# Optimization experiments

Measured on AMD Instinct MI355X. Metric: run time of the kernel, lower is better.

The kernel has to match this reference:

```python
import jax, jax.numpy as jnp
import numpy as np

L, D, H, V, TMAX = 12, 768, 12, 50257, 1024
HD = D // H


def setup_inputs() -> dict:
    key = jax.random.key(0)
    ks = jax.random.split(key, 10)
    std = 0.02
    inp = {
        "input_ids": jax.random.randint(ks[0], (2, 1024), 0, V),
        "wte": jax.random.normal(ks[1], (V, D), jnp.float32) * std,
        "wpe": jax.random.normal(ks[2], (TMAX, D), jnp.float32) * std,
        "ln1_g": jnp.ones((L, D), jnp.float32),
        "ln1_b": jnp.zeros((L, D), jnp.float32),
        "attn_w": jax.random.normal(ks[3], (L, D, 3 * D), jnp.float32) * std,
        "attn_b": jnp.zeros((L, 3 * D), jnp.float32),
        "proj_w": jax.random.normal(ks[4], (L, D, D), jnp.float32) * std,
        "proj_b": jnp.zeros((L, D), jnp.float32),
        "ln2_g": jnp.ones((L, D), jnp.float32),
        "ln2_b": jnp.zeros((L, D), jnp.float32),
        "fc_w": jax.random.normal(ks[5], (L, D, 4 * D), jnp.float32) * std,
        "fc_b": jnp.zeros((L, 4 * D), jnp.float32),
        "fc2_w": jax.random.normal(ks[6], (L, 4 * D, D), jnp.float32) * std,
        "fc2_b": jnp.zeros((L, D), jnp.float32),
        "lnf_g": jnp.ones((D,), jnp.float32),
        "lnf_b": jnp.zeros((D,), jnp.float32),
    }
    return inp


def _layernorm(x, g, b, eps=1e-5):
    m = x.mean(-1, keepdims=True)
    v = ((x - m) ** 2).mean(-1, keepdims=True)
    return (x - m) * jax.lax.rsqrt(v + eps) * g + b


def reference(input_ids, wte, wpe, ln1_g, ln1_b, attn_w, attn_b, proj_w, proj_b,
              ln2_g, ln2_b, fc_w, fc_b, fc2_w, fc2_b, lnf_g, lnf_b):
    B, T = input_ids.shape
    # dropout is identity in eval mode
    x = wte[input_ids] + wpe[:T]  # [B,T,D]
    causal = jnp.tril(jnp.ones((T, T), bool))
    scale = 1.0 / np.sqrt(HD)

    def block(x, p):
        l1g, l1b, aw, ab, pw, pb, l2g, l2b, fw, fb, f2w, f2b = p
        h = _layernorm(x, l1g, l1b)
        qkv = h @ aw + ab  # [B,T,3D]
        q, k, v = jnp.split(qkv, 3, axis=-1)
        q = q.reshape(B, T, H, HD).transpose(0, 2, 1, 3)  # [B,H,T,HD]
        k = k.reshape(B, T, H, HD).transpose(0, 2, 1, 3)
        v = v.reshape(B, T, H, HD).transpose(0, 2, 1, 3)
        att = jnp.einsum('bhqd,bhkd->bhqk', q, k) * scale
        att = jnp.where(causal, att, -jnp.inf)
        att = jax.nn.softmax(att, axis=-1)
        y = jnp.einsum('bhqk,bhkd->bhqd', att, v)
        y = y.transpose(0, 2, 1, 3).reshape(B, T, D)
        x = x + (y @ pw + pb)
        h = _layernorm(x, l2g, l2b)
        h = jax.nn.gelu(h @ fw + fb, approximate=False) @ f2w + f2b
        return x + h, None

    params = (ln1_g, ln1_b, attn_w, attn_b, proj_w, proj_b,
              ln2_g, ln2_b, fc_w, fc_b, fc2_w, fc2_b)
    x, _ = jax.lax.scan(block, x, params)
    x = _layernorm(x, lnf_g, lnf_b)
    logits = x @ wte.T  # tied lm_head, [B,T,V]
    return logits
```

## Files before the change

### kernel.cpp

```cpp
#include <hip/hip_runtime.h>

#define NL 12
#define Dm 768
#define NH 12
#define HD 64
#define NV 50257
#define NB 2
#define NT 1024
#define MROWS (NB * NT)

typedef __attribute__((ext_vector_type(8))) short bf16x8;
typedef __attribute__((ext_vector_type(4))) float f32x4;

__device__ __forceinline__ void split2(float f, unsigned short& h, unsigned short& l) {
    unsigned u = __float_as_uint(f);
    h = (unsigned short)(u >> 16);
    float lf = f - __uint_as_float(u & 0xffff0000u);
    unsigned lu = __float_as_uint(lf);
    l = (unsigned short)((lu + 0x8000u) >> 16);
}

__device__ __forceinline__ float gelu_exact(float v) {
    return 0.5f * v * (1.0f + erff(v * 0.70710678118654752f));
}

union U8 { ushort4 u[2]; bf16x8 v; };

__device__ __forceinline__ bf16x8 ldfrag(const unsigned short* rowp, int lg) {
    U8 t;
    t.u[0] = *(const ushort4*)(rowp + 8 * lg);
    t.u[1] = *(const ushort4*)(rowp + 8 * lg + 4);
    return t.v;
}

__global__ void embed_kernel(const int* __restrict__ ids,
                             const float* __restrict__ wte,
                             const float* __restrict__ wpe,
                             float* __restrict__ x) {
    int row = blockIdx.x;
    int t = row & (NT - 1);
    int id = ids[row];
    const float* src = wte + (size_t)id * Dm;
    const float* pos = wpe + (size_t)t * Dm;
    float* dst = x + (size_t)row * Dm;
    for (int i = threadIdx.x; i < Dm; i += 256)
        dst[i] = src[i] + pos[i];
}

__global__ void ln_kernel(const float* __restrict__ x,
                          const float* __restrict__ g,
                          const float* __restrict__ b,
                          float* __restrict__ out) {
    int row = blockIdx.x;
    int tid = threadIdx.x;
    const float* xr = x + (size_t)row * Dm;
    float v0 = xr[tid];
    float v1 = xr[tid + 256];
    float v2 = xr[tid + 512];
    float s = v0 + v1 + v2;
    #pragma unroll
    for (int off = 32; off; off >>= 1) s += __shfl_xor(s, off);
    __shared__ float red[4];
    __shared__ float red2[4];
    int wid = tid >> 6;
    if ((tid & 63) == 0) red[wid] = s;
    __syncthreads();
    float mean = (red[0] + red[1] + red[2] + red[3]) * (1.0f / Dm);
    float d0 = v0 - mean, d1 = v1 - mean, d2 = v2 - mean;
    float sq = d0 * d0 + d1 * d1 + d2 * d2;
    #pragma unroll
    for (int off = 32; off; off >>= 1) sq += __shfl_xor(sq, off);
    if ((tid & 63) == 0) red2[wid] = sq;
    __syncthreads();
    float var = (red2[0] + red2[1] + red2[2] + red2[3]) * (1.0f / Dm);
    float rstd = rsqrtf(var + 1e-5f);
    float* o = out + (size_t)row * Dm;
    o[tid]       = d0 * rstd * g[tid]       + b[tid];
    o[tid + 256] = d1 * rstd * g[tid + 256] + b[tid + 256];
    o[tid + 512] = d2 * rstd * g[tid + 512] + b[tid + 512];
}

template <int TM, int TN, bool TRANSB>
__global__ __launch_bounds__(256, 3)
void gemm_mfma(const float* __restrict__ A,
               const float* __restrict__ W,
               const float* __restrict__ bias,
               const float* __restrict__ resid,
               float* __restrict__ C,
               int M, int K, int N, int act) {
    constexpr int FRM = TM / 32;
    constexpr int FRN = TN / 32;
    constexpr int CPA = TM / 32;
    constexpr int CPW = TN / 32;
    constexpr int WLD = TN + 4;

    __shared__ __align__(16) unsigned short Ah[TM][36];
    __shared__ __align__(16) unsigned short Al[TM][36];
    __shared__ __align__(16) unsigned short Bh[TN][36];
    __shared__ __align__(16) unsigned short Bl[TN][36];
    __shared__ __align__(16) float Wst[TRANSB ? 4 : 32 * WLD];

    const int tid = threadIdx.x;
    const int lane = tid & 63;
    const int wv = tid >> 6;
    const int wm = wv >> 1, wn = wv & 1;
    const int lr = lane & 15, lg = lane >> 4;
    const int m0 = blockIdx.y * TM;
    const int n0 = blockIdx.x * TN;

    f32x4 acc[FRM][FRN];
    #pragma unroll
    for (int i = 0; i < FRM; ++i)
        #pragma unroll
        for (int j = 0; j < FRN; ++j)
            #pragma unroll
            for (int e = 0; e < 4; ++e) acc[i][j][e] = 0.0f;

    const int ttn = tid & (TN - 1);
    const int tks = (tid / TN) * (TN / 8);

    for (int k0 = 0; k0 < K; k0 += 32) {
        #pragma unroll
        for (int i = 0; i < CPA; ++i) {
            int ci = tid * CPA + i;
            int r = ci >> 3, kc = (ci & 7) << 2;
            float4 v = *(const float4*)(A + (size_t)(m0 + r) * K + k0 + kc);
            ushort4 hh, ll;
            split2(v.x, hh.x, ll.x); split2(v.y, hh.y, ll.y);
            split2(v.z, hh.z, ll.z); split2(v.w, hh.w, ll.w);
            *(ushort4*)&Ah[r][kc] = hh;
            *(ushort4*)&Al[r][kc] = ll;
        }
        if constexpr (TRANSB) {
            #pragma unroll
            for (int i = 0; i < CPW; ++i) {
                int ci = tid * CPW + i;
                int r = ci >> 3, kc = (ci & 7) << 2;
                float4 v = make_float4(0.f, 0.f, 0.f, 0.f);
                if (n0 + r < N)
                    v = *(const float4*)(W + (size_t)(n0 + r) * K + k0 + kc);
                ushort4 hh, ll;
                split2(v.x, hh.x, ll.x); split2(v.y, hh.y, ll.y);
                split2(v.z, hh.z, ll.z); split2(v.w, hh.w, ll.w);
                *(ushort4*)&Bh[r][kc] = hh;
                *(ushort4*)&Bl[r][kc] = ll;
            }
            __syncthreads();
        } else {
            #pragma unroll
            for (int i = 0; i < CPW; ++i) {
                int ci = tid * CPW + i;
                int kk = ci / (TN / 4);
                int nc = (ci % (TN / 4)) << 2;
                *(float4*)&Wst[kk * WLD + nc] =
                    *(const float4*)(W + (size_t)(k0 + kk) * N + n0 + nc);
            }
            __syncthreads();
            #pragma unroll
            for (int j4 = 0; j4 < TN / 32; ++j4) {
                ushort4 hh, ll;
                float w0 = Wst[(tks + j4 * 4 + 0) * WLD + ttn];
                float w1 = Wst[(tks + j4 * 4 + 1) * WLD + ttn];
                float w2 = Wst[(tks + j4 * 4 + 2) * WLD + ttn];
                float w3 = Wst[(tks + j4 * 4 + 3) * WLD + ttn];
                split2(w0, hh.x, ll.x); split2(w1, hh.y, ll.y);
                split2(w2, hh.z, ll.z); split2(w3, hh.w, ll.w);
                *(ushort4*)&Bh[ttn][tks + j4 * 4] = hh;
                *(ushort4*)&Bl[ttn][tks + j4 * 4] = ll;
            }
            __syncthreads();
        }

        bf16x8 afh[FRM], afl[FRM];
        #pragma unroll
        for (int mb = 0; mb < FRM; ++mb) {
            int r = wm * (TM / 2) + mb * 16 + lr;
            afh[mb] = ldfrag(&Ah[r][0], lg);
            afl[mb] = ldfrag(&Al[r][0], lg);
        }
        #pragma unroll
        for (int nb = 0; nb < FRN; ++nb) {
            int cB = wn * (TN / 2) + nb * 16 + lr;
            bf16x8 bfh = ldfrag(&Bh[cB][0], lg);
            bf16x8 bfl = ldfrag(&Bl[cB][0], lg);
            #pragma unroll
            for (int mb = 0; mb < FRM; ++mb) {
                acc[mb][nb] = __builtin_amdgcn_mfma_f32_16x16x32_bf16(afh[mb], bfh, acc[mb][nb], 0, 0, 0);
                acc[mb][nb] = __builtin_amdgcn_mfma_f32_16x16x32_bf16(afl[mb], bfh, acc[mb][nb], 0, 0, 0);
                acc[mb][nb] = __builtin_amdgcn_mfma_f32_16x16x32_bf16(afh[mb], bfl, acc[mb][nb], 0, 0, 0);
            }
        }
        __syncthreads();
    }

    #pragma unroll
    for (int nb = 0; nb < FRN; ++nb) {
        int c = n0 + wn * (TN / 2) + nb * 16 + lr;
        if (c < N) {
            float bv = bias ? bias[c] : 0.0f;
            #pragma unroll
            for (int mb = 0; mb < FRM; ++mb) {
                int rb = m0 + wm * (TM / 2) + mb * 16 + lg * 4;
                #pragma unroll
                for (int i = 0; i < 4; ++i) {
                    size_t idx = (size_t)(rb + i) * N + c;
                    float v = acc[mb][nb][i] + bv;
                    if (act) v = gelu_exact(v);
                    if (resid) v += resid[idx];
                    C[idx] = v;
                }
            }
        }
    }
}

__global__ __launch_bounds__(256, 2)
void attn_mfma(const float* __restrict__ qkv, float* __restrict__ y) {
    __shared__ __align__(16) unsigned short Kh[64][72], Kl[64][72];
    __shared__ __align__(16) unsigned short Vth[64][72], Vtl[64][72];
    __shared__ __align__(16) unsigned short Ph[64][72], Pl[64][72];

    const int tid = threadIdx.x;
    const int lane = tid & 63;
    const int w = tid >> 6;
    const int lr = lane & 15, lg = lane >> 4;
    const int qt = (int)(gridDim.x - 1 - blockIdx.x);
    const int bh = blockIdx.y;
    const int h = bh % NH, b = bh / NH;
    const int q0 = qt * 64;
    const float scale = 0.125f;

    const float* base = qkv + (size_t)b * NT * (3 * Dm);

    bf16x8 qh[2], ql[2];
    {
        const int qrow = q0 + w * 16 + lr;
        const float* qp = base + (size_t)qrow * (3 * Dm) + h * HD + lg * 8;
        #pragma unroll
        for (int ks = 0; ks < 2; ++ks) {
            float4 x0 = *(const float4*)(qp + 32 * ks);
            float4 x1 = *(const float4*)(qp + 32 * ks + 4);
            U8 th, tl;
            split2(x0.x * scale, th.u[0].x, tl.u[0].x);
            split2(x0.y * scale, th.u[0].y, tl.u[0].y);
            split2(x0.z * scale, th.u[0].z, tl.u[0].z);
            split2(x0.w * scale, th.u[0].w, tl.u[0].w);
            split2(x1.x * scale, th.u[1].x, tl.u[1].x);
            split2(x1.y * scale, th.u[1].y, tl.u[1].y);
            split2(x1.z * scale, th.u[1].z, tl.u[1].z);
            split2(x1.w * scale, th.u[1].w, tl.u[1].w);
            qh[ks] = th.v; ql[ks] = tl.v;
        }
    }

    f32x4 yacc[4];
    #pragma unroll
    for (int df = 0; df < 4; ++df)
        #pragma unroll
        for (int e = 0; e < 4; ++e) yacc[df][e] = 0.0f;
    float m[4] = {-1e30f, -1e30f, -1e30f, -1e30f};
    float lsum[4] = {0.0f, 0.0f, 0.0f, 0.0f};

    const int skr = tid >> 4;
    const int sd4 = (tid & 15) << 2;

    for (int kt = 0; kt <= qt; ++kt) {
        const int kt0 = kt * 64;
        __syncthreads();
        #pragma unroll
        for (int i = 0; i < 4; ++i) {
            int kr = i * 16 + skr;
            const float* kp = base + (size_t)(kt0 + kr) * (3 * Dm) + Dm + h * HD + sd4;
            float4 kv = *(const float4*)kp;
            ushort4 hh, ll;
            split2(kv.x, hh.x, ll.x); split2(kv.y, hh.y, ll.y);
            split2(kv.z, hh.z, ll.z); split2(kv.w, hh.w, ll.w);
            *(ushort4*)&Kh[kr][sd4] = hh;
            *(ushort4*)&Kl[kr][sd4] = ll;
            float4 vv = *(const float4*)(kp + Dm);
            unsigned short vh, vl;
            split2(vv.x, vh, vl); Vth[sd4 + 0][kr] = vh; Vtl[sd4 + 0][kr] = vl;
            split2(vv.y, vh, vl); Vth[sd4 + 1][kr] = vh; Vtl[sd4 + 1][kr] = vl;
            split2(vv.z, vh, vl); Vth[sd4 + 2][kr] = vh; Vtl[sd4 + 2][kr] = vl;
            split2(vv.w, vh, vl); Vth[sd4 + 3][kr] = vh; Vtl[sd4 + 3][kr] = vl;
        }
        __syncthreads();

        f32x4 s[4];
        #pragma unroll
        for (int nb = 0; nb < 4; ++nb)
            #pragma unroll
            for (int e = 0; e < 4; ++e) s[nb][e] = 0.0f;
        #pragma unroll
        for (int nb = 0; nb < 4; ++nb) {
            #pragma unroll
            for (int ks = 0; ks < 2; ++ks) {
                bf16x8 kfh = ldfrag(&Kh[nb * 16 + lr][32 * ks], lg);
                bf16x8 kfl = ldfrag(&Kl[nb * 16 + lr][32 * ks], lg);
                s[nb] = __builtin_amdgcn_mfma_f32_16x16x32_bf16(qh[ks], kfh, s[nb], 0, 0, 0);
                s[nb] = __builtin_amdgcn_mfma_f32_16x16x32_bf16(ql[ks], kfh, s[nb], 0, 0, 0);
                s[nb] = __builtin_amdgcn_mfma_f32_16x16x32_bf16(qh[ks], kfl, s[nb], 0, 0, 0);
            }
        }

        if (kt == qt) {
            #pragma unroll
            for (int nb = 0; nb < 4; ++nb) {
                int kg = kt0 + nb * 16 + lr;
                #pragma unroll
                for (int i = 0; i < 4; ++i) {
                    int qg = q0 + w * 16 + 4 * lg + i;
                    if (kg > qg) s[nb][i] = -1e30f;
                }
            }
        }

        float alpha[4];
        #pragma unroll
        for (int i = 0; i < 4; ++i) {
            float mt = fmaxf(fmaxf(s[0][i], s[1][i]), fmaxf(s[2][i], s[3][i]));
            #pragma unroll
            for (int off = 1; off < 16; off <<= 1) mt = fmaxf(mt, __shfl_xor(mt, off));
            float mn = fmaxf(m[i], mt);
            alpha[i] = __expf(m[i] - mn);
            m[i] = mn;
            float rs = 0.0f;
            #pragma unroll
            for (int nb = 0; nb < 4; ++nb) {
                float p = __expf(s[nb][i] - mn);
                s[nb][i] = p;
                rs += p;
            }
            #pragma unroll
            for (int off = 1; off < 16; off <<= 1) rs += __shfl_xor(rs, off);
            lsum[i] = lsum[i] * alpha[i] + rs;
        }

        #pragma unroll
        for (int nb = 0; nb < 4; ++nb) {
            #pragma unroll
            for (int i = 0; i < 4; ++i) {
                unsigned short hh, ll;
                split2(s[nb][i], hh, ll);
                Ph[w * 16 + 4 * lg + i][nb * 16 + lr] = hh;
                Pl[w * 16 + 4 * lg + i][nb * 16 + lr] = ll;
            }
        }
        __syncthreads();

        #pragma unroll
        for (int df = 0; df < 4; ++df)
            #pragma unroll
            for (int i = 0; i < 4; ++i) yacc[df][i] *= alpha[i];
        #pragma unroll
        for (int ks = 0; ks < 2; ++ks) {
            bf16x8 pah = ldfrag(&Ph[w * 16 + lr][32 * ks], lg);
            bf16x8 pal = ldfrag(&Pl[w * 16 + lr][32 * ks], lg);
            #pragma unroll
            for (int df = 0; df < 4; ++df) {
                bf16x8 vfh = ldfrag(&Vth[df * 16 + lr][32 * ks], lg);
                bf16x8 vfl = ldfrag(&Vtl[df * 16 + lr][32 * ks], lg);
                yacc[df] = __builtin_amdgcn_mfma_f32_16x16x32_bf16(pah, vfh, yacc[df], 0, 0, 0);
                yacc[df] = __builtin_amdgcn_mfma_f32_16x16x32_bf16(pal, vfh, yacc[df], 0, 0, 0);
                yacc[df] = __builtin_amdgcn_mfma_f32_16x16x32_bf16(pah, vfl, yacc[df], 0, 0, 0);
            }
        }
    }

    #pragma unroll
    for (int i = 0; i < 4; ++i) {
        float inv = 1.0f / lsum[i];
        int qg = q0 + w * 16 + 4 * lg + i;
        float* yr = y + (size_t)(b * NT + qg) * Dm + h * HD;
        #pragma unroll
        for (int df = 0; df < 4; ++df)
            yr[df * 16 + lr] = yacc[df][i] * inv;
    }
}

extern "C" void kernel_launch(void* const* d_in, const int* in_sizes, int n_in,
                              void* d_out, int out_size, void* d_ws, size_t ws_size,
                              hipStream_t stream) {
    const int*   ids    = (const int*)  d_in[0];
    const float* wte    = (const float*)d_in[1];
    const float* wpe    = (const float*)d_in[2];
    const float* ln1_g  = (const float*)d_in[3];
    const float* ln1_b  = (const float*)d_in[4];
    const float* attn_w = (const float*)d_in[5];
    const float* attn_b = (const float*)d_in[6];
    const float* proj_w = (const float*)d_in[7];
    const float* proj_b = (const float*)d_in[8];
    const float* ln2_g  = (const float*)d_in[9];
    const float* ln2_b  = (const float*)d_in[10];
    const float* fc_w   = (const float*)d_in[11];
    const float* fc_b   = (const float*)d_in[12];
    const float* fc2_w  = (const float*)d_in[13];
    const float* fc2_b  = (const float*)d_in[14];
    const float* lnf_g  = (const float*)d_in[15];
    const float* lnf_b  = (const float*)d_in[16];
    float* out = (float*)d_out;

    float* ws  = (float*)d_ws;
    float* x   = ws;
    float* h   = x   + (size_t)MROWS * Dm;
    float* qkv = h   + (size_t)MROWS * Dm;
    float* y   = qkv + (size_t)MROWS * 3 * Dm;
    float* h4  = y   + (size_t)MROWS * Dm;

    embed_kernel<<<MROWS, 256, 0, stream>>>(ids, wte, wpe, x);

    for (int l = 0; l < NL; ++l) {
        ln_kernel<<<MROWS, 256, 0, stream>>>(x, ln1_g + l * Dm, ln1_b + l * Dm, h);
        gemm_mfma<128, 128, false><<<dim3(3 * Dm / 128, MROWS / 128), 256, 0, stream>>>(
            h, attn_w + (size_t)l * Dm * 3 * Dm, attn_b + (size_t)l * 3 * Dm,
            nullptr, qkv, MROWS, Dm, 3 * Dm, 0);
        attn_mfma<<<dim3(NT / 64, NB * NH), 256, 0, stream>>>(qkv, y);
        gemm_mfma<64, 64, false><<<dim3(Dm / 64, MROWS / 64), 256, 0, stream>>>(
            y, proj_w + (size_t)l * Dm * Dm, proj_b + (size_t)l * Dm,
            x, x, MROWS, Dm, Dm, 0);
        ln_kernel<<<MROWS, 256, 0, stream>>>(x, ln2_g + l * Dm, ln2_b + l * Dm, h);
        gemm_mfma<128, 128, false><<<dim3(4 * Dm / 128, MROWS / 128), 256, 0, stream>>>(
            h, fc_w + (size_t)l * Dm * 4 * Dm, fc_b + (size_t)l * 4 * Dm,
            nullptr, h4, MROWS, Dm, 4 * Dm, 1);
        gemm_mfma<64, 64, false><<<dim3(Dm / 64, MROWS / 64), 256, 0, stream>>>(
            h4, fc2_w + (size_t)l * 4 * Dm * Dm, fc2_b + (size_t)l * Dm,
            x, x, MROWS, 4 * Dm, Dm, 0);
    }

    ln_kernel<<<MROWS, 256, 0, stream>>>(x, lnf_g, lnf_b, h);
    gemm_mfma<128, 128, true><<<dim3((NV + 127) / 128, MROWS / 128), 256, 0, stream>>>(
        h, wte, nullptr, nullptr, out, MROWS, Dm, NV, 0);
}
```

Before: 5.553 ms.

## Pre-split activations and weights into bf16 hi/lo planes outside the GEMM loop

Moves the fp32-to-bf16 hi/lo split out of the GEMM inner loop. Producers (layernorm, attention, the GELU GEMM epilogue) now write split bf16 planes, and weights are pre-split and pre-transposed by separate kernels that run every call. The GEMM then stages ready bf16 tiles straight into shared memory, with no in-loop conversion and no transpose staging. The cost is extra kernels that split all weights each call, plus more workspace traffic from writing and reading hi and lo planes.

```diff
diff --git a/kernel.cpp b/kernel.cpp
--- a/kernel.cpp
+++ b/kernel.cpp
@@ -31,6 +31,39 @@
     t.u[0] = *(const ushort4*)(rowp + 8 * lg);
     t.u[1] = *(const ushort4*)(rowp + 8 * lg + 4);
     return t.v;
+}
+
+__global__ void wtsplit_kernel(const float* __restrict__ W,
+                               unsigned short* __restrict__ Wh,
+                               unsigned short* __restrict__ Wl,
+                               int K, int N) {
+    __shared__ float T[32][33];
+    const int k0 = blockIdx.x * 32, n0 = blockIdx.y * 32;
+    const int t = threadIdx.x;
+    const int r = t >> 3, c4 = (t & 7) << 2;
+    float4 v = *(const float4*)(W + (size_t)(k0 + r) * N + n0 + c4);
+    T[r][c4 + 0] = v.x; T[r][c4 + 1] = v.y; T[r][c4 + 2] = v.z; T[r][c4 + 3] = v.w;
+    __syncthreads();
+    ushort4 hh, ll;
+    split2(T[c4 + 0][r], hh.x, ll.x);
+    split2(T[c4 + 1][r], hh.y, ll.y);
+    split2(T[c4 + 2][r], hh.z, ll.z);
+    split2(T[c4 + 3][r], hh.w, ll.w);
+    *(ushort4*)(Wh + (size_t)(n0 + r) * K + k0 + c4) = hh;
+    *(ushort4*)(Wl + (size_t)(n0 + r) * K + k0 + c4) = ll;
+}
+
+__global__ void wsplit_kernel(const float* __restrict__ W,
+                              unsigned short* __restrict__ Wh,
+                              unsigned short* __restrict__ Wl, size_t n4) {
+    size_t i = (size_t)blockIdx.x * 256 + threadIdx.x;
+    if (i >= n4) return;
+    float4 v = *(const float4*)(W + i * 4);
+    ushort4 hh, ll;
+    split2(v.x, hh.x, ll.x); split2(v.y, hh.y, ll.y);
+    split2(v.z, hh.z, ll.z); split2(v.w, hh.w, ll.w);
+    *(ushort4*)(Wh + i * 4) = hh;
+    *(ushort4*)(Wl + i * 4) = ll;
 }
 
 __global__ void embed_kernel(const int* __restrict__ ids,
@@ -47,10 +80,11 @@
         dst[i] = src[i] + pos[i];
 }
 
-__global__ void ln_kernel(const float* __restrict__ x,
-                          const float* __restrict__ g,
-                          const float* __restrict__ b,
-                          float* __restrict__ out) {
+__global__ void ln_split_kernel(const float* __restrict__ x,
+                                const float* __restrict__ g,
+                                const float* __restrict__ b,
+                                unsigned short* __restrict__ oh,
+                                unsigned short* __restrict__ ol) {
     int row = blockIdx.x;
     int tid = threadIdx.x;
     const float* xr = x + (size_t)row * Dm;
@@ -74,31 +108,33 @@
     __syncthreads();
     float var = (red2[0] + red2[1] + red2[2] + red2[3]) * (1.0f / Dm);
     float rstd = rsqrtf(var + 1e-5f);
-    float* o = out + (size_t)row * Dm;
-    o[tid]       = d0 * rstd * g[tid]       + b[tid];
-    o[tid + 256] = d1 * rstd * g[tid + 256] + b[tid + 256];
-    o[tid + 512] = d2 * rstd * g[tid + 512] + b[tid + 512];
-}
-
-template <int TM, int TN, bool TRANSB>
-__global__ __launch_bounds__(256, 3)
-void gemm_mfma(const float* __restrict__ A,
-               const float* __restrict__ W,
-               const float* __restrict__ bias,
-               const float* __restrict__ resid,
-               float* __restrict__ C,
-               int M, int K, int N, int act) {
+    unsigned short hh, ll;
+    size_t o = (size_t)row * Dm;
+    split2(d0 * rstd * g[tid]       + b[tid],       hh, ll); oh[o + tid]       = hh; ol[o + tid]       = ll;
+    split2(d1 * rstd * g[tid + 256] + b[tid + 256], hh, ll); oh[o + tid + 256] = hh; ol[o + tid + 256] = ll;
+    split2(d2 * rstd * g[tid + 512] + b[tid + 512], hh, ll); oh[o + tid + 512] = hh; ol[o + tid + 512] = ll;
+}
+
+template <int TM, int TN, int BK, bool WSPLIT, bool NGUARD>
+__global__ __launch_bounds__(256, 4)
+void gemm_ps(const unsigned short* __restrict__ Ahg,
+             const unsigned short* __restrict__ Alg,
+             const unsigned short* __restrict__ Whg,
+             const unsigned short* __restrict__ Wlg,
+             const float* __restrict__ Wf,
+             const float* __restrict__ bias,
+             const float* __restrict__ resid,
+             float* __restrict__ C,
+             unsigned short* __restrict__ Ch,
+             unsigned short* __restrict__ Cl,
+             int M, int K, int N, int act) {
+    static_assert(TM * BK == 4096 && TN * BK == 4096, "staging map");
     constexpr int FRM = TM / 32;
     constexpr int FRN = TN / 32;
-    constexpr int CPA = TM / 32;
-    constexpr int CPW = TN / 32;
-    constexpr int WLD = TN + 4;
-
-    __shared__ __align__(16) unsigned short Ah[TM][36];
-    __shared__ __align__(16) unsigned short Al[TM][36];
-    __shared__ __align__(16) unsigned short Bh[TN][36];
-    __shared__ __align__(16) unsigned short Bl[TN][36];
-    __shared__ __align__(16) float Wst[TRANSB ? 4 : 32 * WLD];
+    constexpr int LD = BK + 4;
+
+    __shared__ __align__(16) unsigned short Ahs[TM][LD], Als[TM][LD];
+    __shared__ __align__(16) unsigned short Bhs[TN][LD], Bls[TN][LD];
 
     const int tid = threadIdx.x;
     const int lane = tid & 63;
@@ -108,6 +144,10 @@
     const int m0 = blockIdx.y * TM;
     const int n0 = blockIdx.x * TN;
 
+    constexpr int CPR = BK / 16;
+    const int sr = tid / CPR;
+    const int skc = (tid % CPR) * 16;
+
     f32x4 acc[FRM][FRN];
     #pragma unroll
     for (int i = 0; i < FRM; ++i)
@@ -116,78 +156,77 @@
             #pragma unroll
             for (int e = 0; e < 4; ++e) acc[i][j][e] = 0.0f;
 
-    const int ttn = tid & (TN - 1);
-    const int tks = (tid / TN) * (TN / 8);
-
-    for (int k0 = 0; k0 < K; k0 += 32) {
-        #pragma unroll
-        for (int i = 0; i < CPA; ++i) {
-            int ci = tid * CPA + i;
-            int r = ci >> 3, kc = (ci & 7) << 2;
-            float4 v = *(const float4*)(A + (size_t)(m0 + r) * K + k0 + kc);
-            ushort4 hh, ll;
-            split2(v.x, hh.x, ll.x); split2(v.y, hh.y, ll.y);
-            split2(v.z, hh.z, ll.z); split2(v.w, hh.w, ll.w);
-            *(ushort4*)&Ah[r][kc] = hh;
-            *(ushort4*)&Al[r][kc] = ll;
-        }
-        if constexpr (TRANSB) {
-            #pragma unroll
-            for (int i = 0; i < CPW; ++i) {
-                int ci = tid * CPW + i;
-                int r = ci >> 3, kc = (ci & 7) << 2;
+    for (int k0 = 0; k0 < K; k0 += BK) {
+        {
+            size_t ga = (size_t)(m0 + sr) * K + k0 + skc;
+            uint4 a0 = *(const uint4*)(Ahg + ga);
+            uint4 a1 = *(const uint4*)(Ahg + ga + 8);
+            *(uint2*)&Ahs[sr][skc]      = make_uint2(a0.x, a0.y);
+            *(uint2*)&Ahs[sr][skc + 4]  = make_uint2(a0.z, a0.w);
+            *(uint2*)&Ahs[sr][skc + 8]  = make_uint2(a1.x, a1.y);
+            *(uint2*)&Ahs[sr][skc + 12] = make_uint2(a1.z, a1.w);
+            uint4 l0 = *(const uint4*)(Alg + ga);
+            uint4 l1 = *(const uint4*)(Alg + ga + 8);
+            *(uint2*)&Als[sr][skc]      = make_uint2(l0.x, l0.y);
+            *(uint2*)&Als[sr][skc + 4]  = make_uint2(l0.z, l0.w);
+            *(uint2*)&Als[sr][skc + 8]  = make_uint2(l1.x, l1.y);
+            *(uint2*)&Als[sr][skc + 12] = make_uint2(l1.z, l1.w);
+        }
+        if constexpr (WSPLIT) {
+            bool ok = !NGUARD || (n0 + sr < N);
+            size_t gb = (size_t)(n0 + sr) * K + k0 + skc;
+            uint4 h0 = make_uint4(0, 0, 0, 0), h1 = h0, w0 = h0, w1 = h0;
+            if (ok) {
+                h0 = *(const uint4*)(Whg + gb);
+                h1 = *(const uint4*)(Whg + gb + 8);
+                w0 = *(const uint4*)(Wlg + gb);
+                w1 = *(const uint4*)(Wlg + gb + 8);
+            }
+            *(uint2*)&Bhs[sr][skc]      = make_uint2(h0.x, h0.y);
+            *(uint2*)&Bhs[sr][skc + 4]  = make_uint2(h0.z, h0.w);
+            *(uint2*)&Bhs[sr][skc + 8]  = make_uint2(h1.x, h1.y);
+            *(uint2*)&Bhs[sr][skc + 12] = make_uint2(h1.z, h1.w);
+            *(uint2*)&Bls[sr][skc]      = make_uint2(w0.x, w0.y);
+            *(uint2*)&Bls[sr][skc + 4]  = make_uint2(w0.z, w0.w);
+            *(uint2*)&Bls[sr][skc + 8]  = make_uint2(w1.x, w1.y);
+            *(uint2*)&Bls[sr][skc + 12] = make_uint2(w1.z, w1.w);
+        } else {
+            #pragma unroll
+            for (int i = 0; i < 4; ++i) {
+                int ci = tid * 4 + i;
+                int r = ci / (BK / 4), kc4 = (ci % (BK / 4)) * 4;
                 float4 v = make_float4(0.f, 0.f, 0.f, 0.f);
-                if (n0 + r < N)
-                    v = *(const float4*)(W + (size_t)(n0 + r) * K + k0 + kc);
+                if (!NGUARD || n0 + r < N)
+                    v = *(const float4*)(Wf + (size_t)(n0 + r) * K + k0 + kc4);
                 ushort4 hh, ll;
                 split2(v.x, hh.x, ll.x); split2(v.y, hh.y, ll.y);
                 split2(v.z, hh.z, ll.z); split2(v.w, hh.w, ll.w);
-                *(ushort4*)&Bh[r][kc] = hh;
-                *(ushort4*)&Bl[r][kc] = ll;
-            }
-            __syncthreads();
-        } else {
-            #pragma unroll
-            for (int i = 0; i < CPW; ++i) {
-                int ci = tid * CPW + i;
-                int kk = ci / (TN / 4);
-                int nc = (ci % (TN / 4)) << 2;
-                *(float4*)&Wst[kk * WLD + nc] =
-                    *(const float4*)(W + (size_t)(k0 + kk) * N + n0 + nc);
-            }
-            __syncthreads();
-            #pragma unroll
-            for (int j4 = 0; j4 < TN / 32; ++j4) {
-                ushort4 hh, ll;
-                float w0 = Wst[(tks + j4 * 4 + 0) * WLD + ttn];
-                float w1 = Wst[(tks + j4 * 4 + 1) * WLD + ttn];
-                float w2 = Wst[(tks + j4 * 4 + 2) * WLD + ttn];
-                float w3 = Wst[(tks + j4 * 4 + 3) * WLD + ttn];
-                split2(w0, hh.x, ll.x); split2(w1, hh.y, ll.y);
-                split2(w2, hh.z, ll.z); split2(w3, hh.w, ll.w);
-                *(ushort4*)&Bh[ttn][tks + j4 * 4] = hh;
-                *(ushort4*)&Bl[ttn][tks + j4 * 4] = ll;
-            }
-            __syncthreads();
-        }
-
-        bf16x8 afh[FRM], afl[FRM];
-        #pragma unroll
-        for (int mb = 0; mb < FRM; ++mb) {
-            int r = wm * (TM / 2) + mb * 16 + lr;
-            afh[mb] = ldfrag(&Ah[r][0], lg);
-            afl[mb] = ldfrag(&Al[r][0], lg);
-        }
-        #pragma unroll
-        for (int nb = 0; nb < FRN; ++nb) {
-            int cB = wn * (TN / 2) + nb * 16 + lr;
-            bf16x8 bfh = ldfrag(&Bh[cB][0], lg);
-            bf16x8 bfl = ldfrag(&Bl[cB][0], lg);
+                *(ushort4*)&Bhs[r][kc4] = hh;
+                *(ushort4*)&Bls[r][kc4] = ll;
+            }
+        }
+        __syncthreads();
+
+        #pragma unroll
+        for (int ks = 0; ks < BK / 32; ++ks) {
+            bf16x8 afh[FRM], afl[FRM];
             #pragma unroll
             for (int mb = 0; mb < FRM; ++mb) {
-                acc[mb][nb] = __builtin_amdgcn_mfma_f32_16x16x32_bf16(afh[mb], bfh, acc[mb][nb], 0, 0, 0);
-                acc[mb][nb] = __builtin_amdgcn_mfma_f32_16x16x32_bf16(afl[mb], bfh, acc[mb][nb], 0, 0, 0);
-                acc[mb][nb] = __builtin_amdgcn_mfma_f32_16x16x32_bf16(afh[mb], bfl, acc[mb][nb], 0, 0, 0);
+                int r = wm * (TM / 2) + mb * 16 + lr;
+                afh[mb] = ldfrag(&Ahs[r][32 * ks], lg);
+                afl[mb] = ldfrag(&Als[r][32 * ks], lg);
+            }
+            #pragma unroll
+            for (int nb = 0; nb < FRN; ++nb) {
+                int cB = wn * (TN / 2) + nb * 16 + lr;
+                bf16x8 bfh = ldfrag(&Bhs[cB][32 * ks], lg);
+                bf16x8 bfl = ldfrag(&Bls[cB][32 * ks], lg);
+                #pragma unroll
+                for (int mb = 0; mb < FRM; ++mb) {
+                    acc[mb][nb] = __builtin_amdgcn_mfma_f32_16x16x32_bf16(afh[mb], bfh, acc[mb][nb], 0, 0, 0);
+                    acc[mb][nb] = __builtin_amdgcn_mfma_f32_16x16x32_bf16(afl[mb], bfh, acc[mb][nb], 0, 0, 0);
+                    acc[mb][nb] = __builtin_amdgcn_mfma_f32_16x16x32_bf16(afh[mb], bfl, acc[mb][nb], 0, 0, 0);
+                }
             }
         }
         __syncthreads();
@@ -196,7 +235,7 @@
     #pragma unroll
     for (int nb = 0; nb < FRN; ++nb) {
         int c = n0 + wn * (TN / 2) + nb * 16 + lr;
-        if (c < N) {
+        if (!NGUARD || c < N) {
             float bv = bias ? bias[c] : 0.0f;
             #pragma unroll
             for (int mb = 0; mb < FRM; ++mb) {
@@ -207,7 +246,13 @@
                     float v = acc[mb][nb][i] + bv;
                     if (act) v = gelu_exact(v);
                     if (resid) v += resid[idx];
-                    C[idx] = v;
+                    if (Ch) {
+                        unsigned short hh, ll;
+                        split2(v, hh, ll);
+                        Ch[idx] = hh; Cl[idx] = ll;
+                    } else {
+                        C[idx] = v;
+                    }
                 }
             }
         }
@@ -215,10 +260,12 @@
 }
 
 __global__ __launch_bounds__(256, 2)
-void attn_mfma(const float* __restrict__ qkv, float* __restrict__ y) {
-    __shared__ __align__(16) unsigned short Kh[64][72], Kl[64][72];
-    __shared__ __align__(16) unsigned short Vth[64][72], Vtl[64][72];
-    __shared__ __align__(16) unsigned short Ph[64][72], Pl[64][72];
+void attn_mfma(const float* __restrict__ qkv,
+               unsigned short* __restrict__ yh,
+               unsigned short* __restrict__ yl) {
+    __shared__ __align__(16) unsigned short Kh[64][68], Kl[64][68];
+    __shared__ __align__(16) unsigned short Vth[64][68], Vtl[64][68];
+    __shared__ __align__(16) unsigned short Ph[64][68], Pl[64][68];
 
     const int tid = threadIdx.x;
     const int lane = tid & 63;
@@ -371,10 +418,14 @@
     for (int i = 0; i < 4; ++i) {
         float inv = 1.0f / lsum[i];
         int qg = q0 + w * 16 + 4 * lg + i;
-        float* yr = y + (size_t)(b * NT + qg) * Dm + h * HD;
-        #pragma unroll
-        for (int df = 0; df < 4; ++df)
-            yr[df * 16 + lr] = yacc[df][i] * inv;
+        size_t o = (size_t)(b * NT + qg) * Dm + h * HD;
+        #pragma unroll
+        for (int df = 0; df < 4; ++df) {
+            unsigned short hh, ll;
+            split2(yacc[df][i] * inv, hh, ll);
+            yh[o + df * 16 + lr] = hh;
+            yl[o + df * 16 + lr] = ll;
+        }
     }
 }
 
@@ -400,34 +451,97 @@
     const float* lnf_b  = (const float*)d_in[16];
     float* out = (float*)d_out;
 
-    float* ws  = (float*)d_ws;
-    float* x   = ws;
-    float* h   = x   + (size_t)MROWS * Dm;
-    float* qkv = h   + (size_t)MROWS * Dm;
-    float* y   = qkv + (size_t)MROWS * 3 * Dm;
-    float* h4  = y   + (size_t)MROWS * Dm;
+    typedef unsigned short us;
+    char* base = (char*)d_ws;
+    size_t off = 0;
+    auto alloc = [&](size_t bytes) -> void* {
+        off = (off + 255) & ~(size_t)255;
+        void* r = base + off;
+        off += bytes;
+        return r;
+    };
+
+    float* x    = (float*)alloc((size_t)MROWS * Dm * 4);
+    float* qkvb = (float*)alloc((size_t)MROWS * 3 * Dm * 4);
+    us* hh  = (us*)alloc((size_t)MROWS * Dm * 2);
+    us* hl  = (us*)alloc((size_t)MROWS * Dm * 2);
+    us* yh  = (us*)alloc((size_t)MROWS * Dm * 2);
+    us* yl  = (us*)alloc((size_t)MROWS * Dm * 2);
+    us* h4h = (us*)alloc((size_t)MROWS * 4 * Dm * 2);
+    us* h4l = (us*)alloc((size_t)MROWS * 4 * Dm * 2);
+
+    const size_t EQ = (size_t)Dm * 3 * Dm;
+    const size_t EP = (size_t)Dm * Dm;
+    const size_t EF = (size_t)Dm * 4 * Dm;
+    const size_t EWTE = (size_t)NV * Dm;
+    const size_t full_need = off + 2 * 2 * (EWTE + NL * (EQ + EP + EF + EF)) + 64 * 256;
+    const bool full = ws_size >= full_need;
+
+    us *qWh, *qWl, *pWh, *pWl, *fWh, *fWl, *f2Wh, *f2Wl, *wteh = nullptr, *wtel = nullptr;
+    if (full) {
+        qWh  = (us*)alloc(NL * EQ * 2);  qWl  = (us*)alloc(NL * EQ * 2);
+        pWh  = (us*)alloc(NL * EP * 2);  pWl  = (us*)alloc(NL * EP * 2);
+        fWh  = (us*)alloc(NL * EF * 2);  fWl  = (us*)alloc(NL * EF * 2);
+        f2Wh = (us*)alloc(NL * EF * 2);  f2Wl = (us*)alloc(NL * EF * 2);
+        wteh = (us*)alloc(EWTE * 2);     wtel = (us*)alloc(EWTE * 2);
+        for (int l = 0; l < NL; ++l) {
+            wtsplit_kernel<<<dim3(Dm / 32, 3 * Dm / 32), 256, 0, stream>>>(
+                attn_w + l * EQ, qWh + l * EQ, qWl + l * EQ, Dm, 3 * Dm);
+            wtsplit_kernel<<<dim3(Dm / 32, Dm / 32), 256, 0, stream>>>(
+                proj_w + l * EP, pWh + l * EP, pWl + l * EP, Dm, Dm);
+            wtsplit_kernel<<<dim3(Dm / 32, 4 * Dm / 32), 256, 0, stream>>>(
+                fc_w + l * EF, fWh + l * EF, fWl + l * EF, Dm, 4 * Dm);
+            wtsplit_kernel<<<dim3(4 * Dm / 32, Dm / 32), 256, 0, stream>>>(
+                fc2_w + l * EF, f2Wh + l * EF, f2Wl + l * EF, 4 * Dm, Dm);
+        }
+        size_t n4 = EWTE / 4;
+        wsplit_kernel<<<(unsigned)((n4 + 255) / 256), 256, 0, stream>>>(wte, wteh, wtel, n4);
+    } else {
+        qWh  = (us*)alloc(EQ * 2);  qWl  = (us*)alloc(EQ * 2);
+        pWh  = (us*)alloc(EP * 2);  pWl  = (us*)alloc(EP * 2);
+        fWh  = (us*)alloc(EF * 2);  fWl  = (us*)alloc(EF * 2);
+        f2Wh = (us*)alloc(EF * 2);  f2Wl = (us*)alloc(EF * 2);
+    }
 
     embed_kernel<<<MROWS, 256, 0, stream>>>(ids, wte, wpe, x);
 
     for (int l = 0; l < NL; ++l) {
-        ln_kernel<<<MROWS, 256, 0, stream>>>(x, ln1_g + l * Dm, ln1_b + l * Dm, h);
-        gemm_mfma<128, 128, false><<<dim3(3 * Dm / 128, MROWS / 128), 256, 0, stream>>>(
-            h, attn_w + (size_t)l * Dm * 3 * Dm, attn_b + (size_t)l * 3 * Dm,
-            nullptr, qkv, MROWS, Dm, 3 * Dm, 0);
-        attn_mfma<<<dim3(NT / 64, NB * NH), 256, 0, stream>>>(qkv, y);
-        gemm_mfma<64, 64, false><<<dim3(Dm / 64, MROWS / 64), 256, 0, stream>>>(
-            y, proj_w + (size_t)l * Dm * Dm, proj_b + (size_t)l * Dm,
-            x, x, MROWS, Dm, Dm, 0);
-        ln_kernel<<<MROWS, 256, 0, stream>>>(x, ln2_g + l * Dm, ln2_b + l * Dm, h);
-        gemm_mfma<128, 128, false><<<dim3(4 * Dm / 128, MROWS / 128), 256, 0, stream>>>(
-            h, fc_w + (size_t)l * Dm * 4 * Dm, fc_b + (size_t)l * 4 * Dm,
-            nullptr, h4, MROWS, Dm, 4 * Dm, 1);
-        gemm_mfma<64, 64, false><<<dim3(Dm / 64, MROWS / 64), 256, 0, stream>>>(
-            h4, fc2_w + (size_t)l * 4 * Dm * Dm, fc2_b + (size_t)l * Dm,
-            x, x, MROWS, 4 * Dm, Dm, 0);
-    }
-
-    ln_kernel<<<MROWS, 256, 0, stream>>>(x, lnf_g, lnf_b, h);
-    gemm_mfma<128, 128, true><<<dim3((NV + 127) / 128, MROWS / 128), 256, 0, stream>>>(
-        h, wte, nullptr, nullptr, out, MROWS, Dm, NV, 0);
-}
+        size_t oq = full ? l * EQ : 0, op = full ? l * EP : 0, of = full ? l * EF : 0;
+        if (!full) {
+            wtsplit_kernel<<<dim3(Dm / 32, 3 * Dm / 32), 256, 0, stream>>>(
+                attn_w + l * EQ, qWh, qWl, Dm, 3 * Dm);
+            wtsplit_kernel<<<dim3(Dm / 32, Dm / 32), 256, 0, stream>>>(
+                proj_w + l * EP, pWh, pWl, Dm, Dm);
+            wtsplit_kernel<<<dim3(Dm / 32, 4 * Dm / 32), 256, 0, stream>>>(
+                fc_w + l * EF, fWh, fWl, Dm, 4 * Dm);
+            wtsplit_kernel<<<dim3(4 * Dm / 32, Dm / 32), 256, 0, stream>>>(
+                fc2_w + l * EF, f2Wh, f2Wl, 4 * Dm, Dm);
+        }
+        ln_split_kernel<<<MROWS, 256, 0, stream>>>(x, ln1_g + l * Dm, ln1_b + l * Dm, hh, hl);
+        gemm_ps<128, 128, 32, true, false><<<dim3(3 * Dm / 128, MROWS / 128), 256, 0, stream>>>(
+            hh, hl, qWh + oq, qWl + oq, nullptr, attn_b + (size_t)l * 3 * Dm,
+            nullptr, qkvb, nullptr, nullptr, MROWS, Dm, 3 * Dm, 0);
+        attn_mfma<<<dim3(NT / 64, NB * NH), 256, 0, stream>>>(qkvb, yh, yl);
+        gemm_ps<64, 64, 64, true, false><<<dim3(Dm / 64, MROWS / 64), 256, 0, stream>>>(
+            yh, yl, pWh + op, pWl + op, nullptr, proj_b + (size_t)l * Dm,
+            x, x, nullptr, nullptr, MROWS, Dm, Dm, 0);
+        ln_split_kernel<<<MROWS, 256, 0, stream>>>(x, ln2_g + l * Dm, ln2_b + l * Dm, hh, hl);
+        gemm_ps<128, 128, 32, true, false><<<dim3(4 * Dm / 128, MROWS / 128), 256, 0, stream>>>(
+            hh, hl, fWh + of, fWl + of, nullptr, fc_b + (size_t)l * 4 * Dm,
+            nullptr, nullptr, h4h, h4l, MROWS, Dm, 4 * Dm, 1);
+        gemm_ps<64, 64, 64, true, false><<<dim3(Dm / 64, MROWS / 64), 256, 0, stream>>>(
+            h4h, h4l, f2Wh + of, f2Wl + of, nullptr, fc2_b + (size_t)l * Dm,
+            x, x, nullptr, nullptr, MROWS, 4 * Dm, Dm, 0);
+    }
+
+    ln_split_kernel<<<MROWS, 256, 0, stream>>>(x, lnf_g, lnf_b, hh, hl);
+    if (full) {
+        gemm_ps<128, 128, 32, true, true><<<dim3((NV + 127) / 128, MROWS / 128), 256, 0, stream>>>(
+            hh, hl, wteh, wtel, nullptr, nullptr,
+            nullptr, out, nullptr, nullptr, MROWS, Dm, NV, 0);
+    } else {
+        gemm_ps<128, 128, 32, false, true><<<dim3((NV + 127) / 128, MROWS / 128), 256, 0, stream>>>(
+            hh, hl, nullptr, nullptr, wte, nullptr,
+            nullptr, out, nullptr, nullptr, MROWS, Dm, NV, 0);
+    }
+}
```

New measurement: 4.946 ms. 1.12x faster.
